# Optimization experiments

Measured on AMD Instinct MI355X. Metric: run time of the kernel, lower is better.

The kernel has to match this reference:

```python
import jax, jax.numpy as jnp
import numpy as np

B, S, H, E, K, F = 4, 2048, 1024, 8, 512, 4096


def setup_inputs() -> dict:
    key = jax.random.key(0)
    k0, k1, k2, k3 = jax.random.split(key, 4)
    sc = lambda d: 1.0 / np.sqrt(d).astype(np.float32)
    return {
        "x": jax.random.normal(k0, (B, S, H), jnp.float32),
        "Wg": jax.random.normal(k1, (E, H), jnp.float32) * sc(H),
        "W1": jax.random.normal(k2, (E, H, F), jnp.float32) * sc(H),
        "b1": jnp.zeros((E, F), jnp.float32),
        "W2": jax.random.normal(k3, (E, F, H), jnp.float32) * sc(F),
        "b2": jnp.zeros((E, H), jnp.float32),
    }


def reference(x, Wg, W1, b1, W2, b2):
    # Expert-choice routing MoE (https://arxiv.org/pdf/2202.09368.pdf)
    b, s, h = x.shape
    # gate: [b,s,E] softmax over experts, then each expert picks top-K tokens
    logits = jnp.einsum('bsh,eh->bse', x, Wg)
    Sm = jnp.swapaxes(jax.nn.softmax(logits, axis=-1), 1, 2)   # [b,E,s]
    G, I = jax.lax.top_k(Sm, K)                                 # [b,E,K]
    # gather chosen tokens per expert: [b,E,K,h]
    ex = jnp.take_along_axis(x[:, None, :, :], I[..., None], axis=2)
    # per-expert FFN as grouped GEMMs (vectorized over experts)
    h1 = jax.nn.gelu(jnp.einsum('bekh,ehf->bekf', ex, W1) + b1[None, :, None, :])
    out = jnp.einsum('bekf,efh->bekh', h1, W2) + b2[None, :, None, :]
    out = G[..., None] * out                                    # weight by gate score
    # scatter-add back to token positions (combine)
    new_x = jnp.zeros_like(x).at[jnp.arange(b)[:, None, None], I].add(out)
    return new_x
```

## Files before the change

### kernel.cpp

```cpp
#include <hip/hip_runtime.h>
#include <math.h>
#include <cstdint>

#define Bb 4
#define Ss 2048
#define Hh 1024
#define Ee 8
#define Kk 512
#define Ff 4096

typedef short bf16x8 __attribute__((ext_vector_type(8)));
typedef unsigned short u16x8 __attribute__((ext_vector_type(8)));
typedef float f32x4 __attribute__((ext_vector_type(4)));

__device__ __forceinline__ unsigned short f2bf(float f) {
    unsigned int u = __float_as_uint(f);
    u = (u + 0x7FFFu + ((u >> 16) & 1u)) >> 16;
    return (unsigned short)u;
}

__device__ __forceinline__ void async_copy16(const void* gsrc, void* ldst) {
    auto* g = reinterpret_cast<__attribute__((address_space(1))) void*>(
        reinterpret_cast<uintptr_t>(gsrc));
    auto* l = reinterpret_cast<__attribute__((address_space(3))) void*>(
        (unsigned int)reinterpret_cast<uintptr_t>(ldst));
    __builtin_amdgcn_global_load_lds(g, l, 16, 0, 0);
}

__device__ __forceinline__ float gelu(float v) {
    float v2 = v * v;
    float w = v * fmaf(v2, -0.0713548310f, -1.5957691216f);
    float t = __expf(w);
    return v * __builtin_amdgcn_rcpf(1.0f + t);
}

__global__ __launch_bounds__(256) void cast_kernel(
    const float4* __restrict__ s, ushort4* __restrict__ d)
{
    int i = blockIdx.x * 256 + threadIdx.x;
    float4 v = s[i];
    ushort4 o;
    o.x = f2bf(v.x); o.y = f2bf(v.y); o.z = f2bf(v.z); o.w = f2bf(v.w);
    d[i] = o;
}

__global__ __launch_bounds__(256) void gating_kernel(
    const float* __restrict__ x, const float* __restrict__ wg,
    float* __restrict__ Sm)
{
    int wave = threadIdx.x >> 6;
    int lane = threadIdx.x & 63;
    int token = blockIdx.x * 4 + wave;
    int b = token >> 11, s = token & (Ss - 1);
    const float* xr = x + (size_t)token * Hh;

    double acc[Ee];
#pragma unroll
    for (int e = 0; e < Ee; ++e) acc[e] = 0.0;

    for (int i = 0; i < Hh / 64; ++i) {
        int h = lane + i * 64;
        double xv = (double)xr[h];
#pragma unroll
        for (int e = 0; e < Ee; ++e)
            acc[e] += xv * (double)wg[e * Hh + h];
    }
#pragma unroll
    for (int off = 32; off; off >>= 1) {
#pragma unroll
        for (int e = 0; e < Ee; ++e)
            acc[e] += __shfl_xor(acc[e], off, 64);
    }
    if (lane < Ee) {
        double m = acc[0];
#pragma unroll
        for (int e = 1; e < Ee; ++e) m = acc[e] > m ? acc[e] : m;
        double sum = 0.0;
#pragma unroll
        for (int e = 0; e < Ee; ++e) sum += exp(acc[e] - m);
        double v = exp(acc[lane] - m) / sum;
        Sm[((size_t)(b * Ee + lane)) * Ss + s] = (float)v;
    }
}

__global__ __launch_bounds__(1024) void topk_kernel(
    const float* __restrict__ Sm, int* __restrict__ I, float* __restrict__ G)
{
    __shared__ unsigned long long keys[Ss];
    int be = blockIdx.x;
    const float* row = Sm + (size_t)be * Ss;
    for (int i = threadIdx.x; i < Ss; i += 1024) {
        unsigned int vb = __float_as_uint(row[i]);
        keys[i] = ((unsigned long long)vb << 32) | (unsigned int)(0xFFFFFFFFu - i);
    }
    __syncthreads();
    for (int k = 2; k <= Ss; k <<= 1) {
        for (int j = k >> 1; j > 0; j >>= 1) {
            for (int i = threadIdx.x; i < Ss; i += 1024) {
                int ixj = i ^ j;
                if (ixj > i) {
                    unsigned long long a = keys[i], c = keys[ixj];
                    bool desc = ((i & k) == 0);
                    if (desc ? (a < c) : (a > c)) { keys[i] = c; keys[ixj] = a; }
                }
            }
            __syncthreads();
        }
    }
    if (threadIdx.x < Kk) {
        unsigned long long kk = keys[threadIdx.x];
        I[(size_t)be * Kk + threadIdx.x] = (int)(0xFFFFFFFFu - (unsigned int)(kk & 0xFFFFFFFFu));
        G[(size_t)be * Kk + threadIdx.x] = __uint_as_float((unsigned int)(kk >> 32));
    }
}

__global__ __launch_bounds__(256) void transpose_cast_kernel(
    const float* __restrict__ src, unsigned short* __restrict__ dst, int R, int C)
{
    __shared__ unsigned int tileT[128 * 65];
    int z = blockIdx.z;
    const float* s = src + (size_t)z * R * C;
    unsigned short* d = dst + (size_t)z * R * C;
    int c0 = blockIdx.x * 128, r0 = blockIdx.y * 128;
    int t = threadIdx.x;

    int cq = t & 31;
    int rp0 = t >> 5;
#pragma unroll
    for (int p = 0; p < 8; ++p) {
        int rp = rp0 + p * 8;
        const float* s0 = s + (size_t)(r0 + 2 * rp) * C + c0 + cq * 4;
        float4 a = *(const float4*)s0;
        float4 b = *(const float4*)(s0 + C);
        const float* af = (const float*)&a;
        const float* bf = (const float*)&b;
#pragma unroll
        for (int i = 0; i < 4; ++i) {
            unsigned int lo = f2bf(af[i]);
            unsigned int hi = f2bf(bf[i]);
            tileT[(cq * 4 + i) * 65 + rp] = lo | (hi << 16);
        }
    }
    __syncthreads();

    int cw0 = t >> 4;
    int rseg = t & 15;
#pragma unroll
    for (int p = 0; p < 8; ++p) {
        int c = cw0 + p * 16;
        u16x8 o;
#pragma unroll
        for (int k = 0; k < 4; ++k) {
            unsigned int dd = tileT[c * 65 + rseg * 4 + k];
            o[2 * k]     = (unsigned short)(dd & 0xFFFFu);
            o[2 * k + 1] = (unsigned short)(dd >> 16);
        }
        *(u16x8*)(d + (size_t)(c0 + c) * R + r0 + rseg * 8) = o;
    }
}


#define BAR { asm volatile("" ::: "memory"); __builtin_amdgcn_s_barrier(); asm volatile("" ::: "memory"); }
#define VMW6 asm volatile("s_waitcnt vmcnt(6)" ::: "memory");
#define VMW8 asm volatile("s_waitcnt vmcnt(8)" ::: "memory");
#define PRIO1 __builtin_amdgcn_s_setprio(1);
#define PRIO0 __builtin_amdgcn_s_setprio(0);

#define RD_A(bufi, h) { \
    _Pragma("unroll") for (int i = 0; i < 4; ++i) \
    _Pragma("unroll") for (int ks = 0; ks < 2; ++ks) \
        a[i][ks] = *(const bf16x8*)(ldsc + (bufi)*65536 + (h)*16384 \
            + ((wm64 + i*16 + fr) << 7) + (((ks*4 + quad) ^ fr7) << 4)); }

#define RD_B(bufi, h, B) { \
    _Pragma("unroll") for (int j = 0; j < 2; ++j) \
    _Pragma("unroll") for (int ks = 0; ks < 2; ++ks) \
        B[j][ks] = *(const bf16x8*)(ldsc + (bufi)*65536 + 32768 + (h)*16384 \
            + ((wn32 + j*16 + fr) << 7) + (((ks*4 + quad) ^ fr7) << 4)); }

#define STG_A(bufi, h, kt) { \
    char* _d = ldsm + (bufi)*65536 + (h)*16384 + stoff; \
    async_copy16(srcA[(h)*2+0] + (size_t)(kt)*64, _d); \
    async_copy16(srcA[(h)*2+1] + (size_t)(kt)*64, _d + 1024); }

#define STG_B(bufi, h, kt) { \
    char* _d = ldsm + (bufi)*65536 + 32768 + (h)*16384 + stoff; \
    async_copy16(srcB[(h)*2+0] + (size_t)(kt)*64, _d); \
    async_copy16(srcB[(h)*2+1] + (size_t)(kt)*64, _d + 1024); }

#define MFMA_Q(q, c, B) { \
    _Pragma("unroll") for (int i = 0; i < 4; ++i) \
    _Pragma("unroll") for (int j = 0; j < 2; ++j) \
    _Pragma("unroll") for (int ks = 0; ks < 2; ++ks) \
        acc[q][c][i][j] = __builtin_amdgcn_mfma_f32_16x16x32_bf16( \
            a[i][ks], B[j][ks], acc[q][c][i][j], 0, 0, 0); }

#define GEMM_MAIN(NTILES) \
    f32x4 acc[2][2][4][2] = {}; \
    bf16x8 a[4][2], br0[2][2], br1[2][2]; \
    STG_B(0,0,0) STG_A(0,0,0) STG_B(0,1,0) STG_A(0,1,0) \
    STG_B(1,0,1) STG_A(1,0,1) STG_B(1,1,1) STG_A(1,1,1) \
    VMW8 BAR \
    RD_B(0,0,br0) \
    for (int t2 = 0; t2 < (NTILES); t2 += 2) { \
        const int ka = (t2 + 2 < (NTILES)) ? t2 + 2 : 0; \
        const int kb = (t2 + 3 < (NTILES)) ? t2 + 3 : 0; \
        RD_A(0,0)      STG_B(0,0,ka)      BAR PRIO1 MFMA_Q(0,0,br0) PRIO0 BAR \
        RD_B(0,1,br1)  STG_A(0,0,ka)      BAR PRIO1 MFMA_Q(0,1,br1) PRIO0 BAR \
        RD_A(0,1)      STG_B(0,1,ka) VMW6 BAR PRIO1 MFMA_Q(1,0,br0) PRIO0 BAR \
        RD_B(1,0,br0)  STG_A(0,1,ka)      BAR PRIO1 MFMA_Q(1,1,br1) PRIO0 BAR \
        RD_A(1,0)      STG_B(1,0,kb)      BAR PRIO1 MFMA_Q(0,0,br0) PRIO0 BAR \
        RD_B(1,1,br1)  STG_A(1,0,kb)      BAR PRIO1 MFMA_Q(0,1,br1) PRIO0 BAR \
        RD_A(1,1)      STG_B(1,1,kb) VMW6 BAR PRIO1 MFMA_Q(1,0,br0) PRIO0 BAR \
        RD_B(0,0,br0)  STG_A(1,1,kb)      BAR PRIO1 MFMA_Q(1,1,br1) PRIO0 BAR \
    }

#define GEMM_PREAMBLE \
    const int t = threadIdx.x; \
    const int lane = t & 63, w = t >> 6; \
    const int wm64 = (w >> 2) * 64, wn32 = (w & 3) * 32; \
    const int fr = lane & 15, quad = lane >> 4, fr7 = lane & 7; \
    const int l3 = lane >> 3; \
    const int sc = ((lane & 7) ^ l3) * 8; \
    const int stoff = w * 2048; \
    const int nx = gridDim.x, ny = gridDim.y; \
    const int nwg = nx * ny * gridDim.z; \
    const int flat = blockIdx.x + nx * (blockIdx.y + ny * blockIdx.z); \
    const int lid = (flat & 7) * (nwg >> 3) + (flat >> 3); \
    const int tn = lid % nx; \
    const int _rest = lid / nx; \
    const int by = _rest % ny; \
    const int e = _rest / ny; \
    const int bl = by >> 1, tm = by & 1; \
    const int b = b0 + bl; \
    __shared__ __align__(128) char lds[131072]; \
    const char* ldsc = lds; char* ldsm = lds;

__global__ __launch_bounds__(512, 2) void gemm1_kernel(
    const unsigned short* __restrict__ xb,
    const unsigned short* __restrict__ w1t,
    const float* __restrict__ b1, const int* __restrict__ I,
    unsigned short* __restrict__ h1,
    int b0)
{
    GEMM_PREAMBLE
    const int ib = (b * Ee + e) * Kk + tm * 256;
    const unsigned short* srcA[4];
    const unsigned short* srcB[4];
#pragma unroll
    for (int h = 0; h < 2; ++h)
#pragma unroll
        for (int inst = 0; inst < 2; ++inst) {
            int r = h * 128 + w * 16 + inst * 8 + l3;
            srcA[h * 2 + inst] = xb + ((size_t)(b * Ss + I[ib + r])) * Hh + sc;
            srcB[h * 2 + inst] = w1t + ((size_t)e * Ff + tn * 256 + r) * Hh + sc;
        }

    GEMM_MAIN(Hh / 64)

    float bias[2][2];
#pragma unroll
    for (int c = 0; c < 2; ++c)
#pragma unroll
        for (int j = 0; j < 2; ++j)
            bias[c][j] = b1[(size_t)e * Ff + tn * 256 + c * 128 + wn32 + j * 16 + fr];
#pragma unroll
    for (int q = 0; q < 2; ++q)
#pragma unroll
        for (int i = 0; i < 4; ++i)
#pragma unroll
            for (int r = 0; r < 4; ++r) {
                int m = tm * 256 + q * 128 + wm64 + i * 16 + quad * 4 + r;
                unsigned short* orow = h1 + (((size_t)bl * Ee + e) * Kk + m) * Ff + tn * 256;
#pragma unroll
                for (int c = 0; c < 2; ++c)
#pragma unroll
                    for (int j = 0; j < 2; ++j)
                        orow[c * 128 + wn32 + j * 16 + fr] =
                            f2bf(gelu(acc[q][c][i][j][r] + bias[c][j]));
            }
}

__global__ __launch_bounds__(512, 2) void gemm2_kernel(
    const unsigned short* __restrict__ h1,
    const unsigned short* __restrict__ w2t,
    const float* __restrict__ b2, const int* __restrict__ I, const float* __restrict__ G,
    float* __restrict__ out, int b0)
{
    GEMM_PREAMBLE
    const unsigned short* srcA[4];
    const unsigned short* srcB[4];
#pragma unroll
    for (int h = 0; h < 2; ++h)
#pragma unroll
        for (int inst = 0; inst < 2; ++inst) {
            int r = h * 128 + w * 16 + inst * 8 + l3;
            srcA[h * 2 + inst] = h1 + (((size_t)bl * Ee + e) * Kk + tm * 256 + r) * Ff + sc;
            srcB[h * 2 + inst] = w2t + ((size_t)e * Hh + tn * 256 + r) * Ff + sc;
        }

    GEMM_MAIN(Ff / 64)

    float bias[2][2];
#pragma unroll
    for (int c = 0; c < 2; ++c)
#pragma unroll
        for (int j = 0; j < 2; ++j)
            bias[c][j] = b2[(size_t)e * Hh + tn * 256 + c * 128 + wn32 + j * 16 + fr];
#pragma unroll
    for (int q = 0; q < 2; ++q)
#pragma unroll
        for (int i = 0; i < 4; ++i)
#pragma unroll
            for (int r = 0; r < 4; ++r) {
                int m = tm * 256 + q * 128 + wm64 + i * 16 + quad * 4 + r;
                int slot = (b * Ee + e) * Kk + m;
                float gate = G[slot];
                int tok = I[slot];
                float* orow = out + ((size_t)(b * Ss + tok)) * Hh + tn * 256;
#pragma unroll
                for (int c = 0; c < 2; ++c)
#pragma unroll
                    for (int j = 0; j < 2; ++j)
                        atomicAdd(&orow[c * 128 + wn32 + j * 16 + fr],
                                  (acc[q][c][i][j][r] + bias[c][j]) * gate);
            }
}

extern "C" void kernel_launch(void* const* d_in, const int* in_sizes, int n_in,
                              void* d_out, int out_size, void* d_ws, size_t ws_size,
                              hipStream_t stream) {
    const float* x  = (const float*)d_in[0];
    const float* Wg = (const float*)d_in[1];
    const float* W1 = (const float*)d_in[2];
    const float* b1 = (const float*)d_in[3];
    const float* W2 = (const float*)d_in[4];
    const float* b2 = (const float*)d_in[5];
    float* out = (float*)d_out;

    size_t off = 0;
    char* base = (char*)d_ws;
    auto alloc = [&](size_t bytes) -> void* {
        void* p = base + off;
        off += (bytes + 255) & ~(size_t)255;
        return p;
    };
    float* Sm  = (float*)alloc((size_t)Bb * Ee * Ss * 4);
    int*   I   = (int*)alloc((size_t)Bb * Ee * Kk * 4);
    float* G   = (float*)alloc((size_t)Bb * Ee * Kk * 4);
    unsigned short* W1T = (unsigned short*)alloc((size_t)Ee * Ff * Hh * 2);
    unsigned short* W2T = (unsigned short*)alloc((size_t)Ee * Hh * Ff * 2);
    unsigned short* xb  = (unsigned short*)alloc((size_t)Bb * Ss * Hh * 2);
    size_t fixed = off;
    size_t h1_per_b = (size_t)Ee * Kk * Ff * 2;
    int gb = 4;
    while (gb > 1 && fixed + (size_t)gb * h1_per_b > ws_size) gb >>= 1;
    unsigned short* h1 = (unsigned short*)alloc((size_t)gb * h1_per_b);
    if (off > ws_size) return;

    hipMemsetAsync(d_out, 0, (size_t)out_size * sizeof(float), stream);

    cast_kernel<<<(Bb * Ss * Hh) / 1024, 256, 0, stream>>>((const float4*)x, (ushort4*)xb);
    gating_kernel<<<(Bb * Ss) / 4, 256, 0, stream>>>(x, Wg, Sm);
    topk_kernel<<<Bb * Ee, 1024, 0, stream>>>(Sm, I, G);
    transpose_cast_kernel<<<dim3(Ff / 128, Hh / 128, Ee), 256, 0, stream>>>(W1, W1T, Hh, Ff);
    transpose_cast_kernel<<<dim3(Hh / 128, Ff / 128, Ee), 256, 0, stream>>>(W2, W2T, Ff, Hh);

    for (int g = 0; g < Bb / gb; ++g) {
        gemm1_kernel<<<dim3(Ff / 256, 2 * gb, Ee), 512, 0, stream>>>(xb, W1T, b1, I, h1, g * gb);
        gemm2_kernel<<<dim3(Hh / 256, 2 * gb, Ee), 512, 0, stream>>>(h1, W2T, b2, I, G, out, g * gb);
    }
}
```

Before: 663.5 us.

## Replace atomic scatter-add combine with inverse-index gather combine kernel

```diff
diff --git a/kernel.cpp b/kernel.cpp
--- a/kernel.cpp
+++ b/kernel.cpp
@@ -112,6 +112,36 @@
         I[(size_t)be * Kk + threadIdx.x] = (int)(0xFFFFFFFFu - (unsigned int)(kk & 0xFFFFFFFFu));
         G[(size_t)be * Kk + threadIdx.x] = __uint_as_float((unsigned int)(kk >> 32));
     }
+}
+
+__global__ __launch_bounds__(256) void inv_build_kernel(
+    const int* __restrict__ I, int* __restrict__ cnt, int* __restrict__ inv)
+{
+    int slot = blockIdx.x * 256 + threadIdx.x;
+    int b = slot / (Ee * Kk);
+    int sid = slot - b * (Ee * Kk);
+    int t = I[slot];
+    int p = atomicAdd(&cnt[b * Ss + t], 1);
+    inv[(size_t)(b * Ss + t) * Ee + p] = sid;
+}
+
+__global__ __launch_bounds__(256) void combine_kernel(
+    const float4* __restrict__ Oe, const int* __restrict__ cnt,
+    const int* __restrict__ inv, float4* __restrict__ out, int b0)
+{
+    int blk = blockIdx.x;
+    int bl = blk >> 11, s = blk & (Ss - 1);
+    int tok = (b0 + bl) * Ss + s;
+    int tid = threadIdx.x;
+    int c = cnt[tok];
+    const int* lst = inv + (size_t)tok * Ee;
+    float4 acc = {0.f, 0.f, 0.f, 0.f};
+    for (int i = 0; i < c; ++i) {
+        int sid = lst[i];
+        float4 v = Oe[((size_t)bl * (Ee * Kk) + sid) * (Hh / 4) + tid];
+        acc.x += v.x; acc.y += v.y; acc.z += v.z; acc.w += v.w;
+    }
+    out[(size_t)tok * (Hh / 4) + tid] = acc;
 }
 
 __global__ __launch_bounds__(256) void transpose_cast_kernel(
@@ -284,8 +314,9 @@
 __global__ __launch_bounds__(512, 2) void gemm2_kernel(
     const unsigned short* __restrict__ h1,
     const unsigned short* __restrict__ w2t,
-    const float* __restrict__ b2, const int* __restrict__ I, const float* __restrict__ G,
-    float* __restrict__ out, int b0)
+    const float* __restrict__ b2, const float* __restrict__ G,
+    float* __restrict__ Oe,
+    int b0)
 {
     GEMM_PREAMBLE
     const unsigned short* srcA[4];
@@ -316,14 +347,13 @@
                 int m = tm * 256 + q * 128 + wm64 + i * 16 + quad * 4 + r;
                 int slot = (b * Ee + e) * Kk + m;
                 float gate = G[slot];
-                int tok = I[slot];
-                float* orow = out + ((size_t)(b * Ss + tok)) * Hh + tn * 256;
+                float* orow = Oe + (((size_t)bl * Ee + e) * Kk + m) * Hh + tn * 256;
 #pragma unroll
                 for (int c = 0; c < 2; ++c)
 #pragma unroll
                     for (int j = 0; j < 2; ++j)
-                        atomicAdd(&orow[c * 128 + wn32 + j * 16 + fr],
-                                  (acc[q][c][i][j][r] + bias[c][j]) * gate);
+                        orow[c * 128 + wn32 + j * 16 + fr] =
+                            (acc[q][c][i][j][r] + bias[c][j]) * gate;
             }
 }
 
@@ -348,26 +378,42 @@
     float* Sm  = (float*)alloc((size_t)Bb * Ee * Ss * 4);
     int*   I   = (int*)alloc((size_t)Bb * Ee * Kk * 4);
     float* G   = (float*)alloc((size_t)Bb * Ee * Kk * 4);
+    int*   cnt = (int*)alloc((size_t)Bb * Ss * 4);
+    int*   inv = (int*)alloc((size_t)Bb * Ss * Ee * 4);
+    unsigned short* W2T = (unsigned short*)alloc((size_t)Ee * Hh * Ff * 2);
     unsigned short* W1T = (unsigned short*)alloc((size_t)Ee * Ff * Hh * 2);
-    unsigned short* W2T = (unsigned short*)alloc((size_t)Ee * Hh * Ff * 2);
     unsigned short* xb  = (unsigned short*)alloc((size_t)Bb * Ss * Hh * 2);
     size_t fixed = off;
     size_t h1_per_b = (size_t)Ee * Kk * Ff * 2;
-    int gb = 4;
-    while (gb > 1 && fixed + (size_t)gb * h1_per_b > ws_size) gb >>= 1;
-    unsigned short* h1 = (unsigned short*)alloc((size_t)gb * h1_per_b);
-    if (off > ws_size) return;
-
-    hipMemsetAsync(d_out, 0, (size_t)out_size * sizeof(float), stream);
+    size_t oe_per_b = (size_t)Ee * Kk * Hh * 4;
+    int gb;
+    unsigned short* h1;
+    float* Oe;
+    if (fixed + 4 * h1_per_b <= ws_size) {
+        gb = 4;
+        h1 = (unsigned short*)alloc(4 * h1_per_b);
+        Oe = (float*)W1T;
+    } else {
+        gb = 2;
+        while (gb > 1 && fixed + (size_t)gb * (h1_per_b + oe_per_b) > ws_size) gb >>= 1;
+        h1 = (unsigned short*)alloc((size_t)gb * h1_per_b);
+        Oe = (float*)alloc((size_t)gb * oe_per_b);
+        if (off > ws_size) return;
+    }
+
+    hipMemsetAsync(cnt, 0, (size_t)Bb * Ss * 4, stream);
 
     cast_kernel<<<(Bb * Ss * Hh) / 1024, 256, 0, stream>>>((const float4*)x, (ushort4*)xb);
     gating_kernel<<<(Bb * Ss) / 4, 256, 0, stream>>>(x, Wg, Sm);
     topk_kernel<<<Bb * Ee, 1024, 0, stream>>>(Sm, I, G);
+    inv_build_kernel<<<(Bb * Ee * Kk) / 256, 256, 0, stream>>>(I, cnt, inv);
     transpose_cast_kernel<<<dim3(Ff / 128, Hh / 128, Ee), 256, 0, stream>>>(W1, W1T, Hh, Ff);
     transpose_cast_kernel<<<dim3(Hh / 128, Ff / 128, Ee), 256, 0, stream>>>(W2, W2T, Ff, Hh);
 
     for (int g = 0; g < Bb / gb; ++g) {
         gemm1_kernel<<<dim3(Ff / 256, 2 * gb, Ee), 512, 0, stream>>>(xb, W1T, b1, I, h1, g * gb);
-        gemm2_kernel<<<dim3(Hh / 256, 2 * gb, Ee), 512, 0, stream>>>(h1, W2T, b2, I, G, out, g * gb);
-    }
-}
+        gemm2_kernel<<<dim3(Hh / 256, 2 * gb, Ee), 512, 0, stream>>>(h1, W2T, b2, G, Oe, g * gb);
+        combine_kernel<<<gb * Ss, 256, 0, stream>>>((const float4*)Oe, cnt, inv,
+                                                    (float4*)out, g * gb);
+    }
+}
```

New measurement: 654.7 us. No clear change (-1.3%).
